# Optimization experiments

Hardware: AMD Instinct MI355X
Metric: run time of the kernel (lower is better)

## Reference

```python
import jax, jax.numpy as jnp
import numpy as np

B, S, D, H, F = 16, 1024, 256, 8, 1024
HD = D // H  # head_dim = 32
EPS = 1e-5


def setup_inputs() -> dict:
    key = jax.random.key(0)
    ks = jax.random.split(key, 12)
    sc = 0.02
    return {
        "x":      jax.random.normal(ks[0], (B, S, D), dtype=jnp.float32),
        "gamma1": jnp.ones((S, D), dtype=jnp.float32),
        "beta1":  jnp.zeros((S, D), dtype=jnp.float32),
        "Wqkv":   jax.random.normal(ks[1], (3 * D, D), dtype=jnp.float32) * sc,
        "bqkv":   jnp.zeros((3 * D,), dtype=jnp.float32),
        "Wo":     jax.random.normal(ks[2], (D, D), dtype=jnp.float32) * sc,
        "bo":     jnp.zeros((D,), dtype=jnp.float32),
        "gamma2": jnp.ones((S, D), dtype=jnp.float32),
        "beta2":  jnp.zeros((S, D), dtype=jnp.float32),
        "W1":     jax.random.normal(ks[3], (F, D), dtype=jnp.float32) * sc,
        "b1":     jnp.zeros((F,), dtype=jnp.float32),
        "W2":     jax.random.normal(ks[4], (D, F), dtype=jnp.float32) * sc,
        "b2":     jnp.zeros((D,), dtype=jnp.float32),
    }


def _layernorm_2d(x, gamma, beta):
    # normalizes jointly over the last TWO dims (seq, d_model), biased variance
    mean = jnp.mean(x, axis=(-2, -1), keepdims=True)
    var = jnp.mean((x - mean) ** 2, axis=(-2, -1), keepdims=True)
    y = (x - mean) / jnp.sqrt(var + EPS)
    return gamma * y + beta


def _mha(x, Wqkv, bqkv, Wo, bo):
    b, s, d = x.shape
    qkv = x @ Wqkv.T + bqkv                                  # [B,S,3D]
    qkv = qkv.reshape(b, s, H, 3 * HD).transpose(0, 2, 1, 3)  # [B,H,S,3HD]
    q, k, v = jnp.split(qkv, 3, axis=-1)                      # each [B,H,S,HD]
    scores = jnp.einsum("bhqd,bhkd->bhqk", q, k) / np.sqrt(HD).astype(np.float32)
    attn = jax.nn.softmax(scores, axis=-1)                    # [B,H,S,S]
    values = jnp.einsum("bhqk,bhkd->bhqd", attn, v)           # [B,H,S,HD]
    # NOTE: original torch code reshapes (B,H,S,HD)->(B,S,H*HD) WITHOUT permuting
    # back; we faithfully reproduce that (row-major reshape, same as torch).
    values = values.reshape(b, s, H * HD)
    return values @ Wo.T + bo


def reference(x, gamma1, beta1, Wqkv, bqkv, Wo, bo, gamma2, beta2, W1, b1, W2, b2):
    # pre-norm attention block (dropout is identity at inference)
    h = _layernorm_2d(x, gamma1, beta1)
    h = _mha(h, Wqkv, bqkv, Wo, bo)
    x = x + h
    # pre-norm MLP block
    h = _layernorm_2d(x, gamma2, beta2)
    h = jax.nn.relu(h @ W1.T + b1) @ W2.T + b2
    return x + h
```

## Files before the change

### kernel.cpp

```cpp
#include <hip/hip_runtime.h>
#include <cstdint>
#include <cstddef>

#define SDn (1024*256)

typedef unsigned short u16;
typedef unsigned int   u32;
typedef __bf16 bf16x8 __attribute__((ext_vector_type(8)));
typedef u16    u16x4v __attribute__((ext_vector_type(4)));
typedef u32    u32x4v __attribute__((ext_vector_type(4)));
typedef float  f32x4  __attribute__((ext_vector_type(4)));
typedef float  f32x16 __attribute__((ext_vector_type(16)));

__device__ __forceinline__ u16 f2bf(float f){
  u32 u = __builtin_bit_cast(u32, f);
  u32 r = u + 0x7FFFu + ((u >> 16) & 1u);
  return (u16)(r >> 16);
}
__device__ __forceinline__ float bf2f(u16 v){
  return __builtin_bit_cast(float, (u32)v << 16);
}

#if __has_builtin(__builtin_amdgcn_exp2f)
#define EXP2(x) __builtin_amdgcn_exp2f(x)
#else
#define EXP2(x) exp2f(x)
#endif

__device__ __forceinline__ u32 cvtpk(float a, float b){
  u32 r;
  asm("v_cvt_pk_bf16_f32 %0, %1, %2" : "=v"(r) : "v"(a), "v"(b));
  return r;
}

__device__ __forceinline__ void gll16(const void* g, void* l){
  __builtin_amdgcn_global_load_lds((const __attribute__((address_space(1))) void*)g,
                                   (__attribute__((address_space(3))) void*)l, 16, 0, 0);
}

__global__ void prep(const float* __restrict__ x, float2* __restrict__ part,
                     const float* __restrict__ cw0, const float* __restrict__ cw1,
                     const float* __restrict__ cw2, const float* __restrict__ cw3,
                     u16* __restrict__ co0, u16* __restrict__ co1,
                     u16* __restrict__ co2, u16* __restrict__ co3)
{
  const int bid = blockIdx.x, t = threadIdx.x;
  if (bid < 768){
    int i = bid*256 + t;
    const float* src; u16* dst; int j = i;
    if      (j <  49152){ src = cw0; dst = co0; }
    else if (j <  65536){ src = cw1; dst = co1; j -=  49152; }
    else if (j < 131072){ src = cw2; dst = co2; j -=  65536; }
    else               { src = cw3; dst = co3; j -= 131072; }
    float4 v = ((const float4*)src)[j];
    u16x4v o; o[0]=f2bf(v.x); o[1]=f2bf(v.y); o[2]=f2bf(v.z); o[3]=f2bf(v.w);
    ((u16x4v*)dst)[j] = o;
    return;
  }
  __shared__ float2 red[4];
  const int i = bid - 768;
  const int b = i >> 6, c = i & 63;
  const float4* p = (const float4*)(x + (size_t)b*SDn + (size_t)c*4096);
  float s = 0.f, q = 0.f;
  #pragma unroll
  for (int k=0;k<4;k++){
    float4 v = p[t + k*256];
    s += v.x+v.y+v.z+v.w;
    q += v.x*v.x + v.y*v.y + v.z*v.z + v.w*v.w;
  }
  #pragma unroll
  for (int o=32;o;o>>=1){ s += __shfl_down(s,o); q += __shfl_down(q,o); }
  if ((t & 63) == 0) red[t>>6] = make_float2(s,q);
  __syncthreads();
  if (t == 0){
    float S=0.f,Q=0.f;
    #pragma unroll
    for (int k=0;k<4;k++){ S += red[k].x; Q += red[k].y; }
    part[b*64 + c] = make_float2(S,Q);
  }
}

__global__ void ln_apply(const float* __restrict__ x, const float* __restrict__ gamma,
                         const float* __restrict__ beta, const float2* __restrict__ part,
                         u16* __restrict__ y)
{
  int b = blockIdx.y, c = blockIdx.x, t = threadIdx.x;
  __shared__ float2 stat;
  if (t < 64){
    float2 v = part[b*64 + t];
    float s = v.x, q = v.y;
    #pragma unroll
    for (int o=32;o;o>>=1){ s += __shfl_down(s,o); q += __shfl_down(q,o); }
    if (t == 0){
      float mean = s / (float)SDn;
      float var  = q / (float)SDn - mean*mean;
      stat = make_float2(mean, rsqrtf(var + 1e-5f));
    }
  }
  __syncthreads();
  const float mean = stat.x, rstd = stat.y;
  const size_t off = (size_t)b*SDn + (size_t)c*4096;
  const float4* px = (const float4*)(x + off);
  const float4* pg = (const float4*)(gamma + (size_t)c*4096);
  const float4* pb = (const float4*)(beta  + (size_t)c*4096);
  u16x4v* py = (u16x4v*)(y + off);
  #pragma unroll
  for (int i=0;i<4;i++){
    float4 xv = px[t + i*256];
    float4 gv = pg[t + i*256];
    float4 bv = pb[t + i*256];
    u16x4v o;
    o[0] = f2bf(gv.x*(xv.x-mean)*rstd + bv.x);
    o[1] = f2bf(gv.y*(xv.y-mean)*rstd + bv.y);
    o[2] = f2bf(gv.z*(xv.z-mean)*rstd + bv.z);
    o[3] = f2bf(gv.w*(xv.w-mean)*rstd + bv.w);
    py[t + i*256] = o;
  }
}

__global__ void ln2_apply(const u16* __restrict__ x1b, const float* __restrict__ gamma,
                          const float* __restrict__ beta, const float2* __restrict__ part2,
                          u16* __restrict__ y)
{
  int b = blockIdx.y, c = blockIdx.x, t = threadIdx.x;
  __shared__ float2 stat;
  if (t < 32){
    float2 v = part2[b*32 + t];
    float s = v.x, q = v.y;
    #pragma unroll
    for (int o=16;o;o>>=1){ s += __shfl_down(s,o); q += __shfl_down(q,o); }
    if (t == 0){
      float mean = s / (float)SDn;
      float var  = q / (float)SDn - mean*mean;
      stat = make_float2(mean, rsqrtf(var + 1e-5f));
    }
  }
  __syncthreads();
  const float mean = stat.x, rstd = stat.y;
  const size_t off = (size_t)b*SDn + (size_t)c*4096;
  const u16x4v* px = (const u16x4v*)(x1b + off);
  const float4* pg = (const float4*)(gamma + (size_t)c*4096);
  const float4* pb = (const float4*)(beta  + (size_t)c*4096);
  u16x4v* py = (u16x4v*)(y + off);
  #pragma unroll
  for (int i=0;i<4;i++){
    u16x4v xv = px[t + i*256];
    float4 gv = pg[t + i*256];
    float4 bv = pb[t + i*256];
    u16x4v o;
    o[0] = f2bf(gv.x*(bf2f(xv[0])-mean)*rstd + bv.x);
    o[1] = f2bf(gv.y*(bf2f(xv[1])-mean)*rstd + bv.y);
    o[2] = f2bf(gv.z*(bf2f(xv[2])-mean)*rstd + bv.z);
    o[3] = f2bf(gv.w*(bf2f(xv[3])-mean)*rstd + bv.w);
    py[t + i*256] = o;
  }
}

template<int EPI>
__launch_bounds__(256, 4)
__global__ void gemm128(const u16* __restrict__ A, const u16* __restrict__ W,
                        const float* __restrict__ bias,
                        u16* __restrict__ o0, u16* __restrict__ o1, u16* __restrict__ o2,
                        int K, int N)
{
  __shared__ u16 As[2][4096];
  __shared__ u16 Bs[2][4096];
  const int tid  = threadIdx.x;
  const int lane = tid & 63;
  const int wid  = tid >> 6;
  const int wm = wid >> 1, wn = wid & 1;
  const int g  = lane >> 4;
  const int lr = lane & 15;
  const int m0 = blockIdx.x * 128;
  const int n0 = blockIdx.y * 128;

  f32x4 zf = {0.f,0.f,0.f,0.f};
  f32x4 acc[4][4];
  #pragma unroll
  for (int i=0;i<4;i++)
    #pragma unroll
    for (int j=0;j<4;j++) acc[i][j] = zf;

  const int r0 = tid >> 2, c0 = tid & 3;
  const int cs = c0 ^ ((r0 >> 1) & 3);
  const u16* Ar0 = A + (size_t)(m0 + r0     )*K + cs*8;
  const u16* Ar1 = A + (size_t)(m0 + r0 + 64)*K + cs*8;
  const u16* Wr0 = W + (size_t)(n0 + r0     )*K + cs*8;
  const u16* Wr1 = W + (size_t)(n0 + r0 + 64)*K + cs*8;

  int aoff[4], boff[4];
  #pragma unroll
  for (int m=0;m<4;m++){
    int ra = wm*64 + m*16 + lr;
    aoff[m] = (ra*4 + (g ^ ((ra>>1)&3))) * 8;
    int rb = wn*64 + m*16 + lr;
    boff[m] = (rb*4 + (g ^ ((rb>>1)&3))) * 8;
  }

  auto STAGE = [&](int buf, int k0){
    gll16(Ar0 + k0, &As[buf][tid*8]);
    gll16(Ar1 + k0, &As[buf][(tid+256)*8]);
    gll16(Wr0 + k0, &Bs[buf][tid*8]);
    gll16(Wr1 + k0, &Bs[buf][(tid+256)*8]);
  };

  STAGE(0, 0);
  __syncthreads();
  int cur = 0;
  for (int k0 = 0; k0 < K; k0 += 32){
    if (k0 + 32 < K) STAGE(cur^1, k0 + 32);
    bf16x8 af[4], bfv[4];
    #pragma unroll
    for (int m=0;m<4;m++) af[m]  = *(const bf16x8*)(&As[cur][aoff[m]]);
    #pragma unroll
    for (int n=0;n<4;n++) bfv[n] = *(const bf16x8*)(&Bs[cur][boff[n]]);
    #pragma unroll
    for (int m=0;m<4;m++)
      #pragma unroll
      for (int n=0;n<4;n++)
        acc[m][n] = __builtin_amdgcn_mfma_f32_16x16x32_bf16(af[m], bfv[n], acc[m][n], 0, 0, 0);
    __syncthreads();
    cur ^= 1;
  }

  #pragma unroll
  for (int m=0;m<4;m++){
    const int rowb = m0 + wm*64 + m*16 + g*4;
    #pragma unroll
    for (int n=0;n<4;n++){
      const int col = n0 + wn*64 + n*16 + lr;
      const float bc = bias[col];
      if constexpr (EPI == 0){
        const int hh  = col / 96;
        const int rem = col - hh*96;
        const int which = rem >> 5;
        const int d = rem & 31;
        const int b = rowb >> 10, s0 = rowb & 1023;
        if (which == 2){
          u16x4v pv;
          #pragma unroll
          for (int rr=0;rr<4;rr++) pv[rr] = f2bf(acc[m][n][rr] + bc);
          *(u16x4v*)(o2 + ((size_t)((b*8 + hh)*32 + d))*1024 + s0) = pv;
        } else {
          #pragma unroll
          for (int rr=0;rr<4;rr++){
            float v = acc[m][n][rr] + bc;
            if (which == 0)
              o0[((size_t)((b*8 + hh)*1024 + s0 + rr))*32 + d] = f2bf(v * (0.17677669529663689f * 1.4426950408889634f));
            else
              o1[((size_t)((b*8 + hh)*1024 + s0 + rr))*32 + d] = f2bf(v);
          }
        }
      } else {
        #pragma unroll
        for (int rr=0;rr<4;rr++){
          float v = acc[m][n][rr] + bc;
          o0[(size_t)(rowb + rr) * N + col] = f2bf(v > 0.f ? v : 0.f);
        }
      }
    }
  }
}

template<int MODE>
__launch_bounds__(256, 4)
__global__ void gemm64(const u16* __restrict__ A, const u16* __restrict__ W,
                       const float* __restrict__ bias, const void* __restrict__ resv,
                       void* __restrict__ outv, float2* __restrict__ part2,
                       int K, int N)
{
  __shared__ u16 As[2][2048];
  __shared__ u16 Bs[2][4096];
  __shared__ float2 sred[4];
  const int tid  = threadIdx.x;
  const int lane = tid & 63;
  const int wid  = tid >> 6;
  const int g  = lane >> 4;
  const int lr = lane & 15;
  const int m0 = blockIdx.x * 64;
  const int n0 = blockIdx.y * 128;

  f32x4 zf = {0.f,0.f,0.f,0.f};
  f32x4 acc[4][2];
  #pragma unroll
  for (int i=0;i<4;i++){ acc[i][0]=zf; acc[i][1]=zf; }

  const int r0 = tid >> 2, c0 = tid & 3;
  const int cs = c0 ^ ((r0 >> 1) & 3);
  const u16* Asrc  = A + (size_t)(m0 + r0)*K + cs*8;
  const u16* Wsrc0 = W + (size_t)(n0 + r0     )*K + cs*8;
  const u16* Wsrc1 = W + (size_t)(n0 + r0 + 64)*K + cs*8;

  int aoff[4], boff[2];
  #pragma unroll
  for (int m=0;m<4;m++){
    int ra = m*16 + lr;
    aoff[m] = (ra*4 + (g ^ ((ra>>1)&3))) * 8;
  }
  #pragma unroll
  for (int n=0;n<2;n++){
    int rb = wid*32 + n*16 + lr;
    boff[n] = (rb*4 + (g ^ ((rb>>1)&3))) * 8;
  }

  auto STAGE = [&](int buf, int k0){
    gll16(Asrc  + k0, &As[buf][tid*8]);
    gll16(Wsrc0 + k0, &Bs[buf][tid*8]);
    gll16(Wsrc1 + k0, &Bs[buf][(tid+256)*8]);
  };

  STAGE(0, 0);
  __syncthreads();
  int cur = 0;
  for (int k0 = 0; k0 < K; k0 += 32){
    if (k0 + 32 < K) STAGE(cur^1, k0 + 32);
    bf16x8 af[4], bfv[2];
    #pragma unroll
    for (int m=0;m<4;m++) af[m]  = *(const bf16x8*)(&As[cur][aoff[m]]);
    #pragma unroll
    for (int n=0;n<2;n++) bfv[n] = *(const bf16x8*)(&Bs[cur][boff[n]]);
    #pragma unroll
    for (int m=0;m<4;m++)
      #pragma unroll
      for (int n=0;n<2;n++)
        acc[m][n] = __builtin_amdgcn_mfma_f32_16x16x32_bf16(af[m], bfv[n], acc[m][n], 0, 0, 0);
    __syncthreads();
    cur ^= 1;
  }

  float s = 0.f, q = 0.f;
  #pragma unroll
  for (int m=0;m<4;m++){
    const int rowb = m0 + m*16 + g*4;
    #pragma unroll
    for (int n=0;n<2;n++){
      const int col = n0 + wid*32 + n*16 + lr;
      const float bc = bias[col];
      #pragma unroll
      for (int rr=0;rr<4;rr++){
        size_t idx = (size_t)(rowb + rr) * N + col;
        if constexpr (MODE == 1){
          float v = ((const float*)resv)[idx] + acc[m][n][rr] + bc;
          ((u16*)outv)[idx] = f2bf(v);
          s += v; q += v*v;
        } else {
          float v = bf2f(((const u16*)resv)[idx]) + acc[m][n][rr] + bc;
          ((float*)outv)[idx] = v;
        }
      }
    }
  }

  if constexpr (MODE == 1){
    #pragma unroll
    for (int o=32;o;o>>=1){ s += __shfl_down(s,o); q += __shfl_down(q,o); }
    if (lane == 0) sred[wid] = make_float2(s,q);
    __syncthreads();
    if (tid == 0){
      float S=0.f,Q=0.f;
      #pragma unroll
      for (int k=0;k<4;k++){ S += sred[k].x; Q += sred[k].y; }
      part2[blockIdx.x*2 + blockIdx.y] = make_float2(S,Q);
    }
  }
}

__launch_bounds__(256, 5)
__global__ void attn32(const u16* __restrict__ Q, const u16* __restrict__ Kb,
                       const u16* __restrict__ Vt, u16* __restrict__ vals)
{
  __shared__ u16 Ks[2][4096];
  __shared__ u16 Vs[2][4096];
  const int tid  = threadIdx.x;
  const int lane = tid & 63;
  const int wid  = tid >> 6;
  const int l31  = lane & 31;
  const int l5   = lane >> 5;
  const int bh = blockIdx.x;
  const int q0 = blockIdx.y * 128;
  const size_t base = (size_t)bh * (1024*32);

  const int qrow = q0 + wid*32 + l31;
  const bf16x8 qf0 = *(const bf16x8*)(Q + base + (size_t)qrow*32 + l5*8);
  const bf16x8 qf1 = *(const bf16x8*)(Q + base + (size_t)qrow*32 + 16 + l5*8);

  f32x16 acc = {};
  float lsum = 0.f;

  const int kr = tid >> 2, kc = tid & 3;
  const int vd = tid >> 4, vc = tid & 15;
  const u16* Ksrc0 = Kb + base + (size_t)(kr     )*32 + (kc ^ (kr&3))*8;
  const u16* Ksrc1 = Kb + base + (size_t)(kr + 64)*32 + (kc ^ (kr&3))*8;
  const u16* Vsrc0 = Vt + base + (size_t)(vd     )*1024 + (vc ^ (vd&15))*8;
  const u16* Vsrc1 = Vt + base + (size_t)(vd + 16)*1024 + (vc ^ (vd&15))*8;

  auto STAGE = [&](int buf, int kv0){
    gll16(Ksrc0 + (size_t)kv0*32, &Ks[buf][tid*8]);
    gll16(Ksrc1 + (size_t)kv0*32, &Ks[buf][(tid+256)*8]);
    gll16(Vsrc0 + kv0, &Vs[buf][tid*8]);
    gll16(Vsrc1 + kv0, &Vs[buf][(tid+256)*8]);
  };

  STAGE(0, 0);
  __syncthreads();
  int cur = 0;
  for (int kv0 = 0; kv0 < 1024; kv0 += 128){
    if (kv0 + 128 < 1024) STAGE(cur^1, kv0 + 128);

    #pragma unroll
    for (int G=0; G<4; ++G){
      const u16* ksb = &Ks[cur][(32*G + l31)*32];
      const int sw = l31 & 3;
      bf16x8 kf0 = *(const bf16x8*)(ksb + (((0|l5) ^ sw) << 3));
      bf16x8 kf1 = *(const bf16x8*)(ksb + (((2|l5) ^ sw) << 3));
      f32x16 sf = __builtin_amdgcn_mfma_f32_32x32x16_bf16(kf0, qf0, (f32x16){}, 0, 0, 0);
      sf = __builtin_amdgcn_mfma_f32_32x32x16_bf16(kf1, qf1, sf, 0, 0, 0);

      u32 W[8];
      #pragma unroll
      for (int j=0;j<4;j++){
        float p0 = EXP2(sf[4*j+0]);
        float p1 = EXP2(sf[4*j+1]);
        float p2 = EXP2(sf[4*j+2]);
        float p3 = EXP2(sf[4*j+3]);
        lsum += (p0 + p1) + (p2 + p3);
        W[2*j+0] = cvtpk(p0, p1);
        W[2*j+1] = cvtpk(p2, p3);
      }

      #pragma unroll
      for (int sl=0; sl<2; ++sl){
        u32 a0 = W[4*sl + 0], b0 = W[4*sl + 2];
        u32 a1 = W[4*sl + 1], b1 = W[4*sl + 3];
        asm("v_permlane32_swap_b32 %0, %1" : "+v"(a0), "+v"(b0));
        asm("v_permlane32_swap_b32 %0, %1" : "+v"(a1), "+v"(b1));
        bf16x8 pa = __builtin_bit_cast(bf16x8, (u32x4v){a0, a1, b0, b1});
        const int cp = 4*G + 2*sl + l5;
        bf16x8 vb = *(const bf16x8*)(&Vs[cur][l31*128 + ((cp ^ (l31 & 15)) << 3)]);
        acc = __builtin_amdgcn_mfma_f32_32x32x16_bf16(pa, vb, acc, 0, 0, 0);
      }
    }
    __syncthreads();
    cur ^= 1;
  }

  lsum += __shfl_xor(lsum, 32);
  float inv = 1.0f / lsum;

  const int b = bh >> 3, h = bh & 7;
  #pragma unroll
  for (int r=0;r<16;r++){
    int qloc = (r&3) + 8*(r>>2) + 4*l5;
    float iv = __shfl(inv, qloc);
    int sq = q0 + wid*32 + qloc;
    int srow = h*128 + (sq >> 3);
    vals[((size_t)b*1024 + srow)*256 + (sq&7)*32 + l31] = f2bf(acc[r] * iv);
  }
}

extern "C" void kernel_launch(void* const* d_in, const int* in_sizes, int n_in,
                              void* d_out, int out_size, void* d_ws, size_t ws_size,
                              hipStream_t stream)
{
  const float* x      = (const float*)d_in[0];
  const float* gamma1 = (const float*)d_in[1];
  const float* beta1  = (const float*)d_in[2];
  const float* Wqkv   = (const float*)d_in[3];
  const float* bqkv   = (const float*)d_in[4];
  const float* Wo     = (const float*)d_in[5];
  const float* bo     = (const float*)d_in[6];
  const float* gamma2 = (const float*)d_in[7];
  const float* beta2  = (const float*)d_in[8];
  const float* W1     = (const float*)d_in[9];
  const float* b1     = (const float*)d_in[10];
  const float* W2     = (const float*)d_in[11];
  const float* b2     = (const float*)d_in[12];
  float* out = (float*)d_out;
  char* ws = (char*)d_ws;

  float2* part  = (float2*)(ws + 256);
  float2* part2 = (float2*)(ws + 12288);
  u16* wq   = (u16*)(ws + 16384);
  u16* wo   = (u16*)(ws + 409600);
  u16* w1   = (u16*)(ws + 540672);
  u16* w2   = (u16*)(ws + 1064960);
  u16* hbuf = (u16*)(ws + 1589248);
  u16* qb   = (u16*)(ws + 9977856);
  u16* kb   = (u16*)(ws + 18366464);
  u16* vtb  = (u16*)(ws + 26755072);
  u16* valsb= (u16*)(ws + 35143680);
  u16* midb = (u16*)(ws + 9977856);
  u16* x1b  = (u16*)(ws + 43532288);

  prep<<<1792, 256, 0, stream>>>(x, part, Wqkv, Wo, W1, W2, wq, wo, w1, w2);

  ln_apply<<<dim3(64,16), 256, 0, stream>>>(x, gamma1, beta1, part, hbuf);

  gemm128<0><<<dim3(128,6), 256, 0, stream>>>(hbuf, wq, bqkv, qb, kb, vtb, 256, 768);

  attn32<<<dim3(128,8), 256, 0, stream>>>(qb, kb, vtb, valsb);

  gemm64<1><<<dim3(256,2), 256, 0, stream>>>(valsb, wo, bo, x, x1b, part2, 256, 256);

  ln2_apply<<<dim3(64,16), 256, 0, stream>>>(x1b, gamma2, beta2, part2, hbuf);

  gemm128<2><<<dim3(128,8), 256, 0, stream>>>(hbuf, w1, b1, midb, nullptr, nullptr, 256, 1024);

  gemm64<0><<<dim3(256,2), 256, 0, stream>>>(midb, w2, b2, x1b, out, nullptr, 1024, 256);
}
```

Before: 109.1 us.

## Fuse output projection and residual into attention kernel; cast x to bf16 in prep

```diff
diff --git a/kernel.cpp b/kernel.cpp
--- a/kernel.cpp
+++ b/kernel.cpp
@@ -39,6 +39,7 @@
 }
 
 __global__ void prep(const float* __restrict__ x, float2* __restrict__ part,
+                     u16* __restrict__ xb,
                      const float* __restrict__ cw0, const float* __restrict__ cw1,
                      const float* __restrict__ cw2, const float* __restrict__ cw3,
                      u16* __restrict__ co0, u16* __restrict__ co1,
@@ -60,13 +61,17 @@
   __shared__ float2 red[4];
   const int i = bid - 768;
   const int b = i >> 6, c = i & 63;
-  const float4* p = (const float4*)(x + (size_t)b*SDn + (size_t)c*4096);
+  const size_t off = (size_t)b*SDn + (size_t)c*4096;
+  const float4* p = (const float4*)(x + off);
+  u16x4v* pxb = (u16x4v*)(xb + off);
   float s = 0.f, q = 0.f;
   #pragma unroll
   for (int k=0;k<4;k++){
     float4 v = p[t + k*256];
     s += v.x+v.y+v.z+v.w;
     q += v.x*v.x + v.y*v.y + v.z*v.z + v.w*v.w;
+    u16x4v o; o[0]=f2bf(v.x); o[1]=f2bf(v.y); o[2]=f2bf(v.z); o[3]=f2bf(v.w);
+    pxb[t + k*256] = o;
   }
   #pragma unroll
   for (int o=32;o;o>>=1){ s += __shfl_down(s,o); q += __shfl_down(q,o); }
@@ -80,7 +85,7 @@
   }
 }
 
-__global__ void ln_apply(const float* __restrict__ x, const float* __restrict__ gamma,
+__global__ void ln_apply(const u16* __restrict__ xin, const float* __restrict__ gamma,
                          const float* __restrict__ beta, const float2* __restrict__ part,
                          u16* __restrict__ y)
 {
@@ -100,45 +105,7 @@
   __syncthreads();
   const float mean = stat.x, rstd = stat.y;
   const size_t off = (size_t)b*SDn + (size_t)c*4096;
-  const float4* px = (const float4*)(x + off);
-  const float4* pg = (const float4*)(gamma + (size_t)c*4096);
-  const float4* pb = (const float4*)(beta  + (size_t)c*4096);
-  u16x4v* py = (u16x4v*)(y + off);
-  #pragma unroll
-  for (int i=0;i<4;i++){
-    float4 xv = px[t + i*256];
-    float4 gv = pg[t + i*256];
-    float4 bv = pb[t + i*256];
-    u16x4v o;
-    o[0] = f2bf(gv.x*(xv.x-mean)*rstd + bv.x);
-    o[1] = f2bf(gv.y*(xv.y-mean)*rstd + bv.y);
-    o[2] = f2bf(gv.z*(xv.z-mean)*rstd + bv.z);
-    o[3] = f2bf(gv.w*(xv.w-mean)*rstd + bv.w);
-    py[t + i*256] = o;
-  }
-}
-
-__global__ void ln2_apply(const u16* __restrict__ x1b, const float* __restrict__ gamma,
-                          const float* __restrict__ beta, const float2* __restrict__ part2,
-                          u16* __restrict__ y)
-{
-  int b = blockIdx.y, c = blockIdx.x, t = threadIdx.x;
-  __shared__ float2 stat;
-  if (t < 32){
-    float2 v = part2[b*32 + t];
-    float s = v.x, q = v.y;
-    #pragma unroll
-    for (int o=16;o;o>>=1){ s += __shfl_down(s,o); q += __shfl_down(q,o); }
-    if (t == 0){
-      float mean = s / (float)SDn;
-      float var  = q / (float)SDn - mean*mean;
-      stat = make_float2(mean, rsqrtf(var + 1e-5f));
-    }
-  }
-  __syncthreads();
-  const float mean = stat.x, rstd = stat.y;
-  const size_t off = (size_t)b*SDn + (size_t)c*4096;
-  const u16x4v* px = (const u16x4v*)(x1b + off);
+  const u16x4v* px = (const u16x4v*)(xin + off);
   const float4* pg = (const float4*)(gamma + (size_t)c*4096);
   const float4* pb = (const float4*)(beta  + (size_t)c*4096);
   u16x4v* py = (u16x4v*)(y + off);
@@ -262,16 +229,13 @@
   }
 }
 
-template<int MODE>
 __launch_bounds__(256, 4)
 __global__ void gemm64(const u16* __restrict__ A, const u16* __restrict__ W,
-                       const float* __restrict__ bias, const void* __restrict__ resv,
-                       void* __restrict__ outv, float2* __restrict__ part2,
-                       int K, int N)
+                       const float* __restrict__ bias, const u16* __restrict__ res,
+                       float* __restrict__ outF, int K, int N)
 {
   __shared__ u16 As[2][2048];
   __shared__ u16 Bs[2][4096];
-  __shared__ float2 sred[4];
   const int tid  = threadIdx.x;
   const int lane = tid & 63;
   const int wid  = tid >> 6;
@@ -328,7 +292,6 @@
     cur ^= 1;
   }
 
-  float s = 0.f, q = 0.f;
   #pragma unroll
   for (int m=0;m<4;m++){
     const int rowb = m0 + m*16 + g*4;
@@ -339,45 +302,29 @@
       #pragma unroll
       for (int rr=0;rr<4;rr++){
         size_t idx = (size_t)(rowb + rr) * N + col;
-        if constexpr (MODE == 1){
-          float v = ((const float*)resv)[idx] + acc[m][n][rr] + bc;
-          ((u16*)outv)[idx] = f2bf(v);
-          s += v; q += v*v;
-        } else {
-          float v = bf2f(((const u16*)resv)[idx]) + acc[m][n][rr] + bc;
-          ((float*)outv)[idx] = v;
-        }
+        outF[idx] = bf2f(res[idx]) + acc[m][n][rr] + bc;
       }
     }
   }
-
-  if constexpr (MODE == 1){
-    #pragma unroll
-    for (int o=32;o;o>>=1){ s += __shfl_down(s,o); q += __shfl_down(q,o); }
-    if (lane == 0) sred[wid] = make_float2(s,q);
-    __syncthreads();
-    if (tid == 0){
-      float S=0.f,Q=0.f;
-      #pragma unroll
-      for (int k=0;k<4;k++){ S += sred[k].x; Q += sred[k].y; }
-      part2[blockIdx.x*2 + blockIdx.y] = make_float2(S,Q);
-    }
-  }
-}
-
-__launch_bounds__(256, 5)
-__global__ void attn32(const u16* __restrict__ Q, const u16* __restrict__ Kb,
-                       const u16* __restrict__ Vt, u16* __restrict__ vals)
+}
+
+__launch_bounds__(256, 4)
+__global__ void attn32f(const u16* __restrict__ Q, const u16* __restrict__ Kb,
+                        const u16* __restrict__ Vt, const u16* __restrict__ Wob,
+                        const float* __restrict__ bo, const u16* __restrict__ xb,
+                        u16* __restrict__ x1b, float2* __restrict__ part2)
 {
-  __shared__ u16 Ks[2][4096];
-  __shared__ u16 Vs[2][4096];
+  __shared__ u16 smem[20480];
   const int tid  = threadIdx.x;
   const int lane = tid & 63;
   const int wid  = tid >> 6;
   const int l31  = lane & 31;
   const int l5   = lane >> 5;
+  const int lr   = lane & 15;
+  const int g    = lane >> 4;
   const int bh = blockIdx.x;
-  const int q0 = blockIdx.y * 128;
+  const int qx = blockIdx.y;
+  const int q0 = qx * 128;
   const size_t base = (size_t)bh * (1024*32);
 
   const int qrow = q0 + wid*32 + l31;
@@ -395,10 +342,12 @@
   const u16* Vsrc1 = Vt + base + (size_t)(vd + 16)*1024 + (vc ^ (vd&15))*8;
 
   auto STAGE = [&](int buf, int kv0){
-    gll16(Ksrc0 + (size_t)kv0*32, &Ks[buf][tid*8]);
-    gll16(Ksrc1 + (size_t)kv0*32, &Ks[buf][(tid+256)*8]);
-    gll16(Vsrc0 + kv0, &Vs[buf][tid*8]);
-    gll16(Vsrc1 + kv0, &Vs[buf][(tid+256)*8]);
+    u16* KsB = smem + buf*4096;
+    u16* VsB = smem + 8192 + buf*4096;
+    gll16(Ksrc0 + (size_t)kv0*32, KsB + tid*8);
+    gll16(Ksrc1 + (size_t)kv0*32, KsB + (tid+256)*8);
+    gll16(Vsrc0 + kv0, VsB + tid*8);
+    gll16(Vsrc1 + kv0, VsB + (tid+256)*8);
   };
 
   STAGE(0, 0);
@@ -406,10 +355,12 @@
   int cur = 0;
   for (int kv0 = 0; kv0 < 1024; kv0 += 128){
     if (kv0 + 128 < 1024) STAGE(cur^1, kv0 + 128);
+    const u16* KsC = smem + cur*4096;
+    const u16* VsC = smem + 8192 + cur*4096;
 
     #pragma unroll
     for (int G=0; G<4; ++G){
-      const u16* ksb = &Ks[cur][(32*G + l31)*32];
+      const u16* ksb = KsC + (32*G + l31)*32;
       const int sw = l31 & 3;
       bf16x8 kf0 = *(const bf16x8*)(ksb + (((0|l5) ^ sw) << 3));
       bf16x8 kf1 = *(const bf16x8*)(ksb + (((2|l5) ^ sw) << 3));
@@ -436,7 +387,7 @@
         asm("v_permlane32_swap_b32 %0, %1" : "+v"(a1), "+v"(b1));
         bf16x8 pa = __builtin_bit_cast(bf16x8, (u32x4v){a0, a1, b0, b1});
         const int cp = 4*G + 2*sl + l5;
-        bf16x8 vb = *(const bf16x8*)(&Vs[cur][l31*128 + ((cp ^ (l31 & 15)) << 3)]);
+        bf16x8 vb = *(const bf16x8*)(VsC + l31*128 + ((cp ^ (l31 & 15)) << 3));
         acc = __builtin_amdgcn_mfma_f32_32x32x16_bf16(pa, vb, acc, 0, 0, 0);
       }
     }
@@ -446,15 +397,73 @@
 
   lsum += __shfl_xor(lsum, 32);
   float inv = 1.0f / lsum;
-
-  const int b = bh >> 3, h = bh & 7;
+  u16* T = smem + 16384;
   #pragma unroll
   for (int r=0;r<16;r++){
     int qloc = (r&3) + 8*(r>>2) + 4*l5;
     float iv = __shfl(inv, qloc);
-    int sq = q0 + wid*32 + qloc;
-    int srow = h*128 + (sq >> 3);
-    vals[((size_t)b*1024 + srow)*256 + (sq&7)*32 + l31] = f2bf(acc[r] * iv);
+    int row = wid*4 + (r>>2);
+    int col = ((r&3) + 4*l5)*32 + l31;
+    int ch  = col >> 3;
+    T[row*256 + ((ch ^ row) << 3) + (col & 7)] = f2bf(acc[r] * iv);
+  }
+
+  auto stageWo = [&](int buf, int k0){
+    u16* dst = smem + buf*8192;
+    #pragma unroll
+    for (int j=0;j<4;j++){
+      int ch = tid + j*256;
+      int n = ch >> 2, c = ch & 3;
+      int kcc = c ^ ((n>>1)&3);
+      gll16(Wob + (size_t)n*256 + k0 + kcc*8, dst + ch*8);
+    }
+  };
+  stageWo(0, 0);
+  __syncthreads();
+
+  f32x4 zf4 = {0.f,0.f,0.f,0.f};
+  f32x4 acc2[4] = {zf4, zf4, zf4, zf4};
+  int cw = 0;
+  #pragma unroll
+  for (int kk=0; kk<8; ++kk){
+    if (kk < 7) stageWo(cw^1, (kk+1)*32);
+    bf16x8 af = *(const bf16x8*)(T + lr*256 + (((4*kk + g) ^ lr) << 3));
+    #pragma unroll
+    for (int nt=0; nt<4; ++nt){
+      int n = wid*64 + nt*16 + lr;
+      bf16x8 bw = *(const bf16x8*)(smem + cw*8192 + n*32 + ((g ^ ((n>>1)&3)) << 3));
+      acc2[nt] = __builtin_amdgcn_mfma_f32_16x16x32_bf16(af, bw, acc2[nt], 0, 0, 0);
+    }
+    __syncthreads();
+    cw ^= 1;
+  }
+
+  const int b = bh >> 3, h = bh & 7;
+  const int srow0 = h*128 + qx*16;
+  float ss = 0.f, qq = 0.f;
+  #pragma unroll
+  for (int nt=0; nt<4; ++nt){
+    int col = wid*64 + nt*16 + lr;
+    float bc = bo[col];
+    #pragma unroll
+    for (int rr=0; rr<4; ++rr){
+      int row = g*4 + rr;
+      size_t idx = ((size_t)b*1024 + srow0 + row)*256 + col;
+      float v = bf2f(xb[idx]) + acc2[nt][rr] + bc;
+      x1b[idx] = f2bf(v);
+      ss += v; qq += v*v;
+    }
+  }
+  #pragma unroll
+  for (int o=32;o;o>>=1){ ss += __shfl_down(ss,o); qq += __shfl_down(qq,o); }
+  float2* sred = (float2*)smem;
+  if (lane == 0) sred[wid] = make_float2(ss, qq);
+  __syncthreads();
+  if (tid == 0){
+    float S=0.f, QQ=0.f;
+    #pragma unroll
+    for (int k2=0;k2<4;k2++){ S += sred[k2].x; QQ += sred[k2].y; }
+    part2[b*64 + h*8 + qx] = make_float2(S, QQ);
   }
 }
 
@@ -479,32 +488,30 @@
   char* ws = (char*)d_ws;
 
   float2* part  = (float2*)(ws + 256);
-  float2* part2 = (float2*)(ws + 12288);
-  u16* wq   = (u16*)(ws + 16384);
-  u16* wo   = (u16*)(ws + 409600);
-  u16* w1   = (u16*)(ws + 540672);
-  u16* w2   = (u16*)(ws + 1064960);
-  u16* hbuf = (u16*)(ws + 1589248);
-  u16* qb   = (u16*)(ws + 9977856);
-  u16* kb   = (u16*)(ws + 18366464);
-  u16* vtb  = (u16*)(ws + 26755072);
-  u16* valsb= (u16*)(ws + 35143680);
-  u16* midb = (u16*)(ws + 9977856);
-  u16* x1b  = (u16*)(ws + 43532288);
-
-  prep<<<1792, 256, 0, stream>>>(x, part, Wqkv, Wo, W1, W2, wq, wo, w1, w2);
-
-  ln_apply<<<dim3(64,16), 256, 0, stream>>>(x, gamma1, beta1, part, hbuf);
+  float2* part2 = (float2*)(ws + 8448);
+  u16* wq   = (u16*)(ws + 16896);
+  u16* wo   = (u16*)(ws + 410112);
+  u16* w1   = (u16*)(ws + 541184);
+  u16* w2   = (u16*)(ws + 1065472);
+  u16* hbuf = (u16*)(ws + 1589760);
+  u16* qb   = (u16*)(ws + 9978368);
+  u16* kb   = (u16*)(ws + 18366976);
+  u16* vtb  = (u16*)(ws + 26755584);
+  u16* xb   = (u16*)(ws + 35144192);
+  u16* midb = (u16*)(ws + 9978368);
+  u16* x1b  = (u16*)(ws + 43532800);
+
+  prep<<<1792, 256, 0, stream>>>(x, part, xb, Wqkv, Wo, W1, W2, wq, wo, w1, w2);
+
+  ln_apply<<<dim3(64,16), 256, 0, stream>>>(xb, gamma1, beta1, part, hbuf);
 
   gemm128<0><<<dim3(128,6), 256, 0, stream>>>(hbuf, wq, bqkv, qb, kb, vtb, 256, 768);
 
-  attn32<<<dim3(128,8), 256, 0, stream>>>(qb, kb, vtb, valsb);
-
-  gemm64<1><<<dim3(256,2), 256, 0, stream>>>(valsb, wo, bo, x, x1b, part2, 256, 256);
-
-  ln2_apply<<<dim3(64,16), 256, 0, stream>>>(x1b, gamma2, beta2, part2, hbuf);
+  attn32f<<<dim3(128,8), 256, 0, stream>>>(qb, kb, vtb, wo, bo, xb, x1b, part2);
+
+  ln_apply<<<dim3(64,16), 256, 0, stream>>>(x1b, gamma2, beta2, part2, hbuf);
 
   gemm128<2><<<dim3(128,8), 256, 0, stream>>>(hbuf, w1, b1, midb, nullptr, nullptr, 256, 1024);
 
-  gemm64<0><<<dim3(256,2), 256, 0, stream>>>(midb, w2, b2, x1b, out, nullptr, 1024, 256);
-}
+  gemm64<<<dim3(256,2), 256, 0, stream>>>(midb, w2, b2, x1b, out, 1024, 256);
+}
```

After: 107.6 us, median of 2. No clear change (-1.4%).
